# Optimization experiments

Measured on AMD Instinct MI355X. Metric: run time of the kernel, lower is better.

Reference implementation:

```python
import jax, jax.numpy as jnp
import numpy as np

NUM_HEADS = 12
D_MODEL = 768
D_K = D_MODEL // NUM_HEADS
NEG_INF = -1e9  # matches torch masked_fill value -1000000000.0


def setup_inputs() -> dict:
    key = jax.random.key(0)
    ks = jax.random.split(key, 11)
    B, S, D = 2, 2048, D_MODEL
    s = 1.0 / np.sqrt(D)  # ~ nn.Linear default init scale
    return {
        "q": jax.random.normal(ks[0], (B, S, D), jnp.float32),
        "k": jax.random.normal(ks[1], (B, S, D), jnp.float32),
        "v": jax.random.normal(ks[2], (B, S, D), jnp.float32),
        "mask": jax.random.randint(ks[3], (B, S, S), 0, 2, jnp.int32),
        "Wq": jax.random.normal(ks[4], (D, D), jnp.float32) * s,
        "bq": jax.random.normal(ks[5], (D,), jnp.float32) * s,
        "Wk": jax.random.normal(ks[6], (D, D), jnp.float32) * s,
        "bk": jax.random.normal(ks[7], (D,), jnp.float32) * s,
        "Wv": jax.random.normal(ks[8], (D, D), jnp.float32) * s,
        "bv": jax.random.normal(ks[9], (D,), jnp.float32) * s,
    }


def reference(q, k, v, mask, Wq, bq, Wk, bk, Wv, bv):
    B, S, D = q.shape
    H, dk = NUM_HEADS, D_K
    # torch nn.Linear: x @ W.T + b, then .view(B, H, -1, d_k)
    # NOTE: source uses a raw view (NO transpose) -> plain reshape here, faithfully.
    qh = (q @ Wq.T + bq).reshape(B, H, S, dk)
    kh = (k @ Wk.T + bk).reshape(B, H, S, dk)
    vh = (v @ Wv.T + bv).reshape(B, H, S, dk)
    scores = jnp.einsum("bhqd,bhkd->bhqk", qh, kh) / jnp.sqrt(jnp.asarray(dk, q.dtype))
    # mask.unsqueeze(1): broadcast over heads; masked_fill where mask == 0
    scores = jnp.where(mask[:, None, :, :] == 0, jnp.asarray(NEG_INF, q.dtype), scores)
    attn = jax.nn.softmax(scores, axis=-1)  # dropout = identity (eval mode)
    return jnp.einsum("bhqk,bhkd->bhqd", attn, vh)  # (B, H, S, d_k); no out-proj in source
```

## Files before the change

### kernel.cpp

```cpp
#include <hip/hip_runtime.h>
#include <stdint.h>

#define NUM_B 2
#define SEQ 2048
#define DMODEL 768
#define NHEAD 12
#define DK 64
#define MROWS (NUM_B * SEQ)
#define BHS (NUM_B * NHEAD * SEQ)

typedef __attribute__((ext_vector_type(4))) float f32x4;
typedef __attribute__((ext_vector_type(16))) float f32x16;
typedef __attribute__((ext_vector_type(8))) short bf16x8;
typedef __attribute__((ext_vector_type(8))) unsigned short us8;
typedef __attribute__((ext_vector_type(4))) unsigned short us4;
typedef __attribute__((ext_vector_type(4))) unsigned int u32x4;
typedef unsigned short u16;
typedef unsigned int u32;
typedef unsigned long long u64;

__device__ __forceinline__ u16 to_bf16(float f) {
  u32 u = __builtin_bit_cast(u32, f);
  u += 0x7FFFu + ((u >> 16) & 1u);
  return (u16)(u >> 16);
}

__device__ __forceinline__ float bf16_to_f32(u16 u) {
  return __builtin_bit_cast(float, ((u32)u) << 16);
}

__device__ __forceinline__ u32 cvt_pk_bf16(float lo, float hi) {
  u32 r;
  asm("v_cvt_pk_bf16_f32 %0, %1, %2" : "=v"(r) : "v"(lo), "v"(hi));
  return r;
}

__device__ __forceinline__ float fexp2(float x) {
  float r;
  asm("v_exp_f32 %0, %1" : "=v"(r) : "v"(x));
  return r;
}

__device__ __forceinline__ int sext_bit(u32 src, int pos) {
#if __has_builtin(__builtin_amdgcn_sbfe)
  return __builtin_amdgcn_sbfe((int)src, pos, 1);
#else
  return ((int)(src << (31 - pos))) >> 31;
#endif
}

__device__ __forceinline__ void gload_lds16(const u16* g, u16* l) {
#pragma clang diagnostic push
#pragma clang diagnostic ignored "-Waddress-space-conversion"
  __builtin_amdgcn_global_load_lds((const __attribute__((address_space(1))) u32*)g,
                                   (__attribute__((address_space(3))) u32*)l, 16, 0, 0);
#pragma clang diagnostic pop
}

__global__ void cvt_pack(const float* s0, const float* s1, const float* s2,
                         const float* s3, const float* s4, const float* s5,
                         const int* __restrict__ mask,
                         u16* d0, u16* d1, u16* d2, u16* d3, u16* d4, u16* d5,
                         u64* __restrict__ bits, int nbig, int nsmall) {
  int y = blockIdx.y;
  if (y == 6) {
    int base = blockIdx.x * (16 * 256) + threadIdx.x;
#pragma unroll
    for (int it = 0; it < 16; ++it) {
      int i = base + it * 256;
      u64 bm = __ballot(mask[i] != 0);
      if ((threadIdx.x & 63) == 0) {
        int word = (i >> 6) & 31;
        int s = (i >> 11) & 2047;
        int b = i >> 22;
        bits[((size_t)b * 32 + word) * 2048 + s] = bm;
      }
    }
    return;
  }
  const float* src; u16* dst; int n8;
  if (y == 0)      { src = s0; dst = d0; n8 = nbig; }
  else if (y == 1) { src = s1; dst = d1; n8 = nbig; }
  else if (y == 2) { src = s2; dst = d2; n8 = nbig; }
  else if (y == 3) { src = s3; dst = d3; n8 = nsmall; }
  else if (y == 4) { src = s4; dst = d4; n8 = nsmall; }
  else             { src = s5; dst = d5; n8 = nsmall; }
  int i = blockIdx.x * blockDim.x + threadIdx.x;
  if (i >= n8) return;
  const f32x4* p = reinterpret_cast<const f32x4*>(src) + (size_t)i * 2;
  f32x4 lo = p[0], hi = p[1];
  us8 r;
  r[0] = to_bf16(lo[0]); r[1] = to_bf16(lo[1]); r[2] = to_bf16(lo[2]); r[3] = to_bf16(lo[3]);
  r[4] = to_bf16(hi[0]); r[5] = to_bf16(hi[1]); r[6] = to_bf16(hi[2]); r[7] = to_bf16(hi[3]);
  *(reinterpret_cast<us8*>(dst) + i) = r;
}

__global__ __launch_bounds__(256) void proj_gemm(
    const u16* __restrict__ X0, const u16* __restrict__ X1, const u16* __restrict__ X2,
    const u16* __restrict__ W0, const u16* __restrict__ W1, const u16* __restrict__ W2,
    const float* __restrict__ b0, const float* __restrict__ b1, const float* __restrict__ b2,
    u16* __restrict__ o0, u16* __restrict__ o1, u16* __restrict__ o2) {
  __shared__ u16 As[2][8192];
  __shared__ u16 Bs[2][4096];

  int lin = blockIdx.x + 384 * blockIdx.y;
  int wid = (lin & 7) * 144 + (lin >> 3);
  int y = wid / 384;
  int r384 = wid % 384;
  int bm = r384 / 12, bn = r384 % 12;

  const u16* X; const u16* W; const float* bias; u16* out;
  if (y == 0)      { X = X0; W = W0; bias = b0; out = o0; }
  else if (y == 1) { X = X1; W = W1; bias = b1; out = o1; }
  else             { X = X2; W = W2; bias = b2; out = o2; }
  float osc = (y == 0) ? 0.18033688011112042f : 1.0f;

  int tid = threadIdx.x, w = tid >> 6, l = tid & 63;
  int g = l >> 4, c = l & 15;
  int m0 = bm * 128, n0 = bn * 64;
  int wm = w >> 1, wn = w & 1;

  int srow = l >> 3;
  int cg = (l & 7) ^ srow;

  f32x4 acc[4][2] = {};

  auto stage = [&](int kt, int buf) {
    int k0 = kt * 64;
#pragma unroll
    for (int i = 0; i < 4; ++i) {
      int row = i * 32 + w * 8 + srow;
      gload_lds16(X + (size_t)(m0 + row) * DMODEL + k0 + cg * 8, &As[buf][(i * 256 + w * 64) * 8]);
    }
#pragma unroll
    for (int i = 0; i < 2; ++i) {
      int row = i * 32 + w * 8 + srow;
      gload_lds16(W + (size_t)(n0 + row) * DMODEL + k0 + cg * 8, &Bs[buf][(i * 256 + w * 64) * 8]);
    }
  };

  stage(0, 0);
  __syncthreads();

  for (int kt = 0; kt < 12; ++kt) {
    int cur = kt & 1;
    if (kt < 11) stage(kt + 1, cur ^ 1);
#pragma unroll
    for (int kk = 0; kk < 2; ++kk) {
      bf16x8 av[4], bv[2];
#pragma unroll
      for (int m = 0; m < 4; ++m) {
        int row = wm * 64 + m * 16 + c;
        av[m] = *(const bf16x8*)&As[cur][row * 64 + ((kk * 32 + g * 8) ^ ((row & 7) << 3))];
      }
#pragma unroll
      for (int n = 0; n < 2; ++n) {
        int row = wn * 32 + n * 16 + c;
        bv[n] = *(const bf16x8*)&Bs[cur][row * 64 + ((kk * 32 + g * 8) ^ ((row & 7) << 3))];
      }
#pragma unroll
      for (int m = 0; m < 4; ++m)
#pragma unroll
        for (int n = 0; n < 2; ++n)
          acc[m][n] = __builtin_amdgcn_mfma_f32_16x16x32_bf16(av[m], bv[n], acc[m][n], 0, 0, 0);
    }
    __syncthreads();
  }
#pragma unroll
  for (int n = 0; n < 2; ++n) {
    int gcol = n0 + wn * 32 + n * 16 + c;
    float bvv = bias[gcol];
#pragma unroll
    for (int m = 0; m < 4; ++m) {
      int grow0 = m0 + wm * 64 + m * 16 + g * 4;
#pragma unroll
      for (int r = 0; r < 4; ++r)
        out[(size_t)(grow0 + r) * DMODEL + gcol] = to_bf16((acc[m][n][r] + bvv) * osc);
    }
  }
}

__global__ __launch_bounds__(256) void transposeV(const u16* __restrict__ vh,
                                                  u16* __restrict__ vhT) {
  __shared__ u16 T[64][72];
  int bh = blockIdx.y;
  int s0 = blockIdx.x * 64;
  int tid = threadIdx.x;
#pragma unroll
  for (int it = 0; it < 2; ++it) {
    int cch = it * 256 + tid;
    int r = cch >> 3, dc = (cch & 7) * 8;
    us8 v = *(const us8*)(vh + ((size_t)bh * 2048 + s0 + r) * 64 + dc);
#pragma unroll
    for (int j = 0; j < 8; ++j) T[dc + j][r] = v[j];
  }
  __syncthreads();
#pragma unroll
  for (int it = 0; it < 2; ++it) {
    int cch = it * 256 + tid;
    int d = cch >> 3, sc = (cch & 7) * 8;
    us8 v = *(const us8*)&T[d][sc];
    *(us8*)(vhT + ((size_t)bh * 64 + d) * 2048 + s0 + sc) = v;
  }
}

__global__ __launch_bounds__(256) void attn32(
    const u16* __restrict__ qh, const u16* __restrict__ kh, const u16* __restrict__ vt,
    const u64* __restrict__ mbt, float* __restrict__ po0, u16* __restrict__ po1,
    u16* __restrict__ po2, u16* __restrict__ po3, float* __restrict__ pl) {
  __shared__ u16 K0[4096], V0[4096], K1[4096], V1[4096];

  int tid = threadIdx.x, w = tid >> 6, l = tid & 63;
  int q = l & 31, hi = l >> 5;

  int lin = blockIdx.x + 16 * (blockIdx.y + 12 * blockIdx.z);
  int wid = (lin & 7) * 192 + (lin >> 3);
  int qb = wid & 15;
  int rest = wid >> 4;
  int h = rest % 12;
  int z = rest / 12;
  int strip = z & 3, b = z >> 2;
  int kbase = strip * 512;
  size_t hb = (size_t)(b * NHEAD + h) * SEQ * DK;
  int qrow = qb * 128 + w * 32 + q;

  bf16x8 qf[4];
#pragma unroll
  for (int s = 0; s < 4; ++s)
    qf[s] = *(const bf16x8*)(qh + hb + (size_t)qrow * DK + s * 16 + hi * 8);

  f32x16 o0 = {}, o1 = {};
  float l_run = 0.f;

  int idx0 = w * 64 + l;
  int r0s = idx0 >> 3;
  int sc0 = ((idx0 & 7) ^ (r0s & 7)) * 8;
  const u16* kS = kh + hb + (size_t)(kbase + r0s) * DK + sc0;
  const u16* vS = vt + hb + (size_t)r0s * SEQ + kbase + sc0;
  const u64* mp = mbt + ((size_t)b * 32 + strip * 8) * SEQ + qrow;

  auto stage = [&](int t, u16* Kd, u16* Vd) {
    const u16* kp = kS + (size_t)t * (64 * DK);
    const u16* vp = vS + t * 64;
    gload_lds16(kp,            Kd + w * 512);
    gload_lds16(kp + 32 * DK,  Kd + 2048 + w * 512);
    gload_lds16(vp,            Vd + w * 512);
    gload_lds16(vp + 32 * SEQ, Vd + 2048 + w * 512);
  };

  int ofA[4];
#pragma unroll
  for (int s = 0; s < 4; ++s)
    ofA[s] = q * 64 + (((2 * s + hi) ^ (q & 7)) * 8);

  auto computeHalf = [&](const u16* Kc, const u16* Vc, u32 mm, int kb) {
    const int roff = kb * 2048;
    f32x16 s = {};
#pragma unroll
    for (int ss = 0; ss < 4; ++ss) {
      bf16x8 kf = *(const bf16x8*)(Kc + ofA[ss] + roff);
      s = __builtin_amdgcn_mfma_f32_32x32x16_bf16(kf, qf[ss], s, 0, 0, 0);
    }

    float rs0 = 0.f, rs1 = 0.f, rs2 = 0.f, rs3 = 0.f;
#pragma unroll
    for (int r = 0; r < 16; ++r) {
      const int p = (r & 3) + 8 * (r >> 2);
      float e = fexp2(s[r]);
      int km = sext_bit(mm, p);
      e = __builtin_bit_cast(float, __builtin_bit_cast(int, e) & km);
      s[r] = e;
      if ((r & 3) == 0) rs0 += e;
      else if ((r & 3) == 1) rs1 += e;
      else if ((r & 3) == 2) rs2 += e;
      else rs3 += e;
    }
    l_run += (rs0 + rs1) + (rs2 + rs3);

#pragma unroll
    for (int hf = 0; hf < 2; ++hf) {
      int ks = kb * 2 + hf;
      u32 A0 = cvt_pk_bf16(s[8 * hf + 0], s[8 * hf + 1]);
      u32 A1 = cvt_pk_bf16(s[8 * hf + 2], s[8 * hf + 3]);
      u32 B0 = cvt_pk_bf16(s[8 * hf + 4], s[8 * hf + 5]);
      u32 B1 = cvt_pk_bf16(s[8 * hf + 6], s[8 * hf + 7]);
      asm("v_permlane32_swap_b32 %0, %1" : "+v"(A0), "+v"(B0));
      asm("v_permlane32_swap_b32 %0, %1" : "+v"(A1), "+v"(B1));
      u32x4 fw;
      fw[0] = A0; fw[1] = A1; fw[2] = B0; fw[3] = B1;
      bf16x8 pa = __builtin_bit_cast(bf16x8, fw);
      bf16x8 v0 = *(const bf16x8*)(Vc + ofA[ks]);
      bf16x8 v1 = *(const bf16x8*)(Vc + ofA[ks] + 2048);
      o0 = __builtin_amdgcn_mfma_f32_32x32x16_bf16(pa, v0, o0, 0, 0, 0);
      o1 = __builtin_amdgcn_mfma_f32_32x32x16_bf16(pa, v1, o1, 0, 0, 0);
    }
  };

  auto compute = [&](const u16* Kc, const u16* Vc, u64 mcur) {
    computeHalf(Kc, Vc, (u32)(mcur >> (4 * hi)), 0);
    computeHalf(Kc, Vc, (u32)((mcur >> 32) >> (4 * hi)), 1);
  };

  stage(0, K0, V0);
  u64 mcur = mp[0];
  __syncthreads();

  for (int tt = 0; tt < 4; ++tt) {
    const int t0 = 2 * tt;
    u64 mnext = mp[(size_t)(t0 + 1) * SEQ];
    stage(t0 + 1, K1, V1);
    compute(K0, V0, mcur);
    __syncthreads();
    mcur = mnext;
    if (tt < 3) {
      mnext = mp[(size_t)(t0 + 2) * SEQ];
      stage(t0 + 2, K0, V0);
    }
    compute(K1, V1, mcur);
    __syncthreads();
    mcur = mnext;
  }

  l_run += __shfl_xor(l_run, 32);
  if (strip == 0) {
#pragma unroll
    for (int r = 0; r < 16; ++r) {
      int crow = (r & 3) + 8 * (r >> 2) + 4 * hi;
      float invl = __builtin_amdgcn_rcpf(__shfl(l_run, crow));
      int row = qb * 128 + w * 32 + crow;
      po0[hb + (size_t)row * DK + q]      = o0[r] * invl;
      po0[hb + (size_t)row * DK + 32 + q] = o1[r] * invl;
    }
  } else {
    u16* oo = (strip == 1) ? po1 : (strip == 2) ? po2 : po3;
#pragma unroll
    for (int r = 0; r < 16; ++r) {
      int crow = (r & 3) + 8 * (r >> 2) + 4 * hi;
      float invl = __builtin_amdgcn_rcpf(__shfl(l_run, crow));
      int row = qb * 128 + w * 32 + crow;
      oo[hb + (size_t)row * DK + q]      = to_bf16(o0[r] * invl);
      oo[hb + (size_t)row * DK + 32 + q] = to_bf16(o1[r] * invl);
    }
  }
  if (hi == 0)
    pl[(size_t)strip * BHS + (size_t)(b * NHEAD + h) * SEQ + qrow] = l_run;
}

__global__ __launch_bounds__(256) void combine_kernel(
    const float* __restrict__ po0, const u16* __restrict__ po1,
    const u16* __restrict__ po2, const u16* __restrict__ po3,
    const float* __restrict__ pl, float* __restrict__ out) {
  int i = blockIdx.x * 256 + threadIdx.x;
  int row = i >> 4;
  float l0 = pl[row], l1 = pl[BHS + row], l2 = pl[2 * BHS + row], l3 = pl[3 * BHS + row];
  float inv = 1.f / (l0 + l1 + l2 + l3);
  f32x4 a = ((const f32x4*)po0)[i];
  us4 b1 = ((const us4*)po1)[i];
  us4 b2 = ((const us4*)po2)[i];
  us4 b3 = ((const us4*)po3)[i];
  f32x4 acc;
#pragma unroll
  for (int j = 0; j < 4; ++j)
    acc[j] = a[j] * l0 + bf16_to_f32(b1[j]) * l1 + bf16_to_f32(b2[j]) * l2 +
             bf16_to_f32(b3[j]) * l3;
  ((f32x4*)out)[i] = acc * inv;
}

extern "C" void kernel_launch(void* const* d_in, const int* in_sizes, int n_in,
                              void* d_out, int out_size, void* d_ws, size_t ws_size,
                              hipStream_t stream) {
  const float* q    = (const float*)d_in[0];
  const float* k    = (const float*)d_in[1];
  const float* v    = (const float*)d_in[2];
  const int*   mask = (const int*)d_in[3];
  const float* Wq   = (const float*)d_in[4];
  const float* bq   = (const float*)d_in[5];
  const float* Wk   = (const float*)d_in[6];
  const float* bk   = (const float*)d_in[7];
  const float* Wv   = (const float*)d_in[8];
  const float* bv   = (const float*)d_in[9];

  char* ws = (char*)d_ws;
  const size_t szX = (size_t)MROWS * DMODEL * 2;
  const size_t szW = (size_t)DMODEL * DMODEL * 2;
  u16* xq  = (u16*)(ws);
  u16* xk  = (u16*)(ws + szX);
  u16* xv  = (u16*)(ws + 2 * szX);
  u16* wqb = (u16*)(ws + 3 * szX);
  u16* wkb = (u16*)(ws + 3 * szX + szW);
  u16* wvb = (u16*)(ws + 3 * szX + 2 * szW);
  u16* qh  = (u16*)(ws + 3 * szX + 3 * szW);
  u16* kh  = (u16*)(ws + 4 * szX + 3 * szW);
  u16* vh  = (u16*)(ws + 5 * szX + 3 * szW);
  u64* mb  = (u64*)(ws + 6 * szX + 3 * szW);

  u16*   po1b = (u16*)(ws);
  u16*   po2b = (u16*)(ws + szX);
  u16*   vhT  = (u16*)(ws + 2 * szX);
  float* pl   = (float*)(ws + 3 * szX);
  u16*   po3b = (u16*)(ws + 5 * szX + 3 * szW);
  float* po0  = (float*)d_out;

  const int nbig = (MROWS * DMODEL) / 8;
  const int nsmall = (DMODEL * DMODEL) / 8;

  cvt_pack<<<dim3(2048, 7), 256, 0, stream>>>(q, k, v, Wq, Wk, Wv, mask,
                                              xq, xk, xv, wqb, wkb, wvb, mb,
                                              nbig, nsmall);
  proj_gemm<<<dim3(384, 3), 256, 0, stream>>>(
      xq, xk, xv, wqb, wkb, wvb, bq, bk, bv, qh, kh, vh);
  transposeV<<<dim3(32, 24), 256, 0, stream>>>(vh, vhT);
  attn32<<<dim3(16, 12, 8), 256, 0, stream>>>(qh, kh, vhT, mb, po0, po1b, po2b, po3b, pl);
  combine_kernel<<<(BHS * 16) / 256, 256, 0, stream>>>(po0, po1b, po2b, po3b, pl, (float*)d_out);
}
```

Before: 102.5 us.

## Drop split-K attention strips and combine kernel; process full key range per block

Removes the four-way key-range split of the attention kernel and the separate combine kernel. Each block now loops over all 32 key tiles and writes normalized fp32 output directly, avoiding partial-output writes in bf16/fp32, the l-sum buffer and an extra launch. In exchange the grid shrinks from 1536 to 384 blocks, which lowers parallelism and occupancy on a large GPU and lengthens each block's serial loop. The bf16 rounding of partial outputs also goes away.

New measurement: 103.0 us. No clear change (+0.5%).

```diff
diff --git a/kernel.cpp b/kernel.cpp
--- a/kernel.cpp
+++ b/kernel.cpp
@@ -13,7 +13,6 @@
 typedef __attribute__((ext_vector_type(16))) float f32x16;
 typedef __attribute__((ext_vector_type(8))) short bf16x8;
 typedef __attribute__((ext_vector_type(8))) unsigned short us8;
-typedef __attribute__((ext_vector_type(4))) unsigned short us4;
 typedef __attribute__((ext_vector_type(4))) unsigned int u32x4;
 typedef unsigned short u16;
 typedef unsigned int u32;
@@ -23,10 +22,6 @@
   u32 u = __builtin_bit_cast(u32, f);
   u += 0x7FFFu + ((u >> 16) & 1u);
   return (u16)(u >> 16);
-}
-
-__device__ __forceinline__ float bf16_to_f32(u16 u) {
-  return __builtin_bit_cast(float, ((u32)u) << 16);
 }
 
 __device__ __forceinline__ u32 cvt_pk_bf16(float lo, float hi) {
@@ -206,21 +201,18 @@
 
 __global__ __launch_bounds__(256) void attn32(
     const u16* __restrict__ qh, const u16* __restrict__ kh, const u16* __restrict__ vt,
-    const u64* __restrict__ mbt, float* __restrict__ po0, u16* __restrict__ po1,
-    u16* __restrict__ po2, u16* __restrict__ po3, float* __restrict__ pl) {
+    const u64* __restrict__ mbt, float* __restrict__ outp) {
   __shared__ u16 K0[4096], V0[4096], K1[4096], V1[4096];
 
   int tid = threadIdx.x, w = tid >> 6, l = tid & 63;
   int q = l & 31, hi = l >> 5;
 
   int lin = blockIdx.x + 16 * (blockIdx.y + 12 * blockIdx.z);
-  int wid = (lin & 7) * 192 + (lin >> 3);
+  int wid = (lin & 7) * 48 + (lin >> 3);
   int qb = wid & 15;
   int rest = wid >> 4;
   int h = rest % 12;
-  int z = rest / 12;
-  int strip = z & 3, b = z >> 2;
-  int kbase = strip * 512;
+  int b = rest / 12;
   size_t hb = (size_t)(b * NHEAD + h) * SEQ * DK;
   int qrow = qb * 128 + w * 32 + q;
 
@@ -235,9 +227,9 @@
   int idx0 = w * 64 + l;
   int r0s = idx0 >> 3;
   int sc0 = ((idx0 & 7) ^ (r0s & 7)) * 8;
-  const u16* kS = kh + hb + (size_t)(kbase + r0s) * DK + sc0;
-  const u16* vS = vt + hb + (size_t)r0s * SEQ + kbase + sc0;
-  const u64* mp = mbt + ((size_t)b * 32 + strip * 8) * SEQ + qrow;
+  const u16* kS = kh + hb + (size_t)r0s * DK + sc0;
+  const u16* vS = vt + hb + (size_t)r0s * SEQ + sc0;
+  const u64* mp = mbt + (size_t)b * 32 * SEQ + qrow;
 
   auto stage = [&](int t, u16* Kd, u16* Vd) {
     const u16* kp = kS + (size_t)t * (64 * DK);
@@ -305,14 +297,14 @@
   u64 mcur = mp[0];
   __syncthreads();
 
-  for (int tt = 0; tt < 4; ++tt) {
+  for (int tt = 0; tt < 16; ++tt) {
     const int t0 = 2 * tt;
     u64 mnext = mp[(size_t)(t0 + 1) * SEQ];
     stage(t0 + 1, K1, V1);
     compute(K0, V0, mcur);
     __syncthreads();
     mcur = mnext;
-    if (tt < 3) {
+    if (tt < 15) {
       mnext = mp[(size_t)(t0 + 2) * SEQ];
       stage(t0 + 2, K0, V0);
     }
@@ -322,48 +314,14 @@
   }
 
   l_run += __shfl_xor(l_run, 32);
-  if (strip == 0) {
-#pragma unroll
-    for (int r = 0; r < 16; ++r) {
-      int crow = (r & 3) + 8 * (r >> 2) + 4 * hi;
-      float invl = __builtin_amdgcn_rcpf(__shfl(l_run, crow));
-      int row = qb * 128 + w * 32 + crow;
-      po0[hb + (size_t)row * DK + q]      = o0[r] * invl;
-      po0[hb + (size_t)row * DK + 32 + q] = o1[r] * invl;
-    }
-  } else {
-    u16* oo = (strip == 1) ? po1 : (strip == 2) ? po2 : po3;
-#pragma unroll
-    for (int r = 0; r < 16; ++r) {
-      int crow = (r & 3) + 8 * (r >> 2) + 4 * hi;
-      float invl = __builtin_amdgcn_rcpf(__shfl(l_run, crow));
-      int row = qb * 128 + w * 32 + crow;
-      oo[hb + (size_t)row * DK + q]      = to_bf16(o0[r] * invl);
-      oo[hb + (size_t)row * DK + 32 + q] = to_bf16(o1[r] * invl);
-    }
-  }
-  if (hi == 0)
-    pl[(size_t)strip * BHS + (size_t)(b * NHEAD + h) * SEQ + qrow] = l_run;
-}
-
-__global__ __launch_bounds__(256) void combine_kernel(
-    const float* __restrict__ po0, const u16* __restrict__ po1,
-    const u16* __restrict__ po2, const u16* __restrict__ po3,
-    const float* __restrict__ pl, float* __restrict__ out) {
-  int i = blockIdx.x * 256 + threadIdx.x;
-  int row = i >> 4;
-  float l0 = pl[row], l1 = pl[BHS + row], l2 = pl[2 * BHS + row], l3 = pl[3 * BHS + row];
-  float inv = 1.f / (l0 + l1 + l2 + l3);
-  f32x4 a = ((const f32x4*)po0)[i];
-  us4 b1 = ((const us4*)po1)[i];
-  us4 b2 = ((const us4*)po2)[i];
-  us4 b3 = ((const us4*)po3)[i];
-  f32x4 acc;
-#pragma unroll
-  for (int j = 0; j < 4; ++j)
-    acc[j] = a[j] * l0 + bf16_to_f32(b1[j]) * l1 + bf16_to_f32(b2[j]) * l2 +
-             bf16_to_f32(b3[j]) * l3;
-  ((f32x4*)out)[i] = acc * inv;
+#pragma unroll
+  for (int r = 0; r < 16; ++r) {
+    int crow = (r & 3) + 8 * (r >> 2) + 4 * hi;
+    float invl = __builtin_amdgcn_rcpf(__shfl(l_run, crow));
+    int row = qb * 128 + w * 32 + crow;
+    outp[hb + (size_t)row * DK + q]      = o0[r] * invl;
+    outp[hb + (size_t)row * DK + 32 + q] = o1[r] * invl;
+  }
 }
 
 extern "C" void kernel_launch(void* const* d_in, const int* in_sizes, int n_in,
@@ -393,13 +351,7 @@
   u16* kh  = (u16*)(ws + 4 * szX + 3 * szW);
   u16* vh  = (u16*)(ws + 5 * szX + 3 * szW);
   u64* mb  = (u64*)(ws + 6 * szX + 3 * szW);
-
-  u16*   po1b = (u16*)(ws);
-  u16*   po2b = (u16*)(ws + szX);
-  u16*   vhT  = (u16*)(ws + 2 * szX);
-  float* pl   = (float*)(ws + 3 * szX);
-  u16*   po3b = (u16*)(ws + 5 * szX + 3 * szW);
-  float* po0  = (float*)d_out;
+  u16* vhT = (u16*)(ws + 2 * szX);
 
   const int nbig = (MROWS * DMODEL) / 8;
   const int nsmall = (DMODEL * DMODEL) / 8;
@@ -410,6 +362,5 @@
   proj_gemm<<<dim3(384, 3), 256, 0, stream>>>(
       xq, xk, xv, wqb, wkb, wvb, bq, bk, bv, qh, kh, vh);
   transposeV<<<dim3(32, 24), 256, 0, stream>>>(vh, vhT);
-  attn32<<<dim3(16, 12, 8), 256, 0, stream>>>(qh, kh, vhT, mb, po0, po1b, po2b, po3b, pl);
-  combine_kernel<<<(BHS * 16) / 256, 256, 0, stream>>>(po0, po1b, po2b, po3b, pl, (float*)d_out);
-}
+  attn32<<<dim3(16, 12, 2), 256, 0, stream>>>(qh, kh, vhT, mb, (float*)d_out);
+}
```
